# Optimization experiments

Hardware: AMD Instinct MI355X
Metric: run time of the kernel (lower is better)

Reference implementation:

```python
import jax, jax.numpy as jnp
import numpy as np

WINDOW = 2
OUT = 256


def setup_inputs() -> dict:
    key = jax.random.key(0)
    k1, k2 = jax.random.split(key)
    B, S, I = 8, 4096, 256
    x = jax.random.normal(k1, (B, S, I), dtype=jnp.float32)
    # fc: Linear(window*input -> 2*out*3)
    fan_in = WINDOW * I
    W_fc = jax.random.normal(k2, (2 * OUT * 3, fan_in), dtype=jnp.float32) / np.sqrt(fan_in)
    b_fc = jnp.zeros((2 * OUT * 3,), dtype=jnp.float32)
    return {"x": x, "W_fc": W_fc, "b_fc": b_fc}


def _forget_mult(z_t, f_t, reverse):
    # z_t, f_t: (S, B, O) time-major. c[t] = f[t]*c[prev] + (1-f[t])*z[t], c init 0.
    def step(c, fz):
        f, z = fz
        c = f * c + (1.0 - f) * z
        return c, c

    _, cs = jax.lax.scan(step, jnp.zeros_like(z_t[0]), (f_t, z_t), reverse=reverse)
    return cs  # (S, B, O)


def reference(x, W_fc, b_fc):
    B, S, I = x.shape
    pad = max(WINDOW - 1, 1)
    # stride(): left zero-pad then window of consecutive timesteps, flattened
    xp = jnp.pad(x, ((0, 0), (pad, 0), (0, 0)))
    win = jnp.concatenate([xp[:, k:k + S, :] for k in range(WINDOW)], axis=-1)  # (B,S,W*I)
    g = jnp.einsum('bsi,gi->bsg', win, W_fc) + b_fc  # (B,S,6*O)
    z, f, o = jnp.split(g, 3, axis=2)  # each (B,S,2*O)
    z = jnp.tanh(z)
    f = jax.nn.sigmoid(f)
    # time-major per-direction views
    zt = jnp.swapaxes(z.reshape(B, S, 2, OUT), 0, 1)  # (S,B,2,O)
    ft = jnp.swapaxes(f.reshape(B, S, 2, OUT), 0, 1)
    c_fwd = _forget_mult(zt[:, :, 0], ft[:, :, 0], reverse=False)
    c_bwd = _forget_mult(zt[:, :, 1], ft[:, :, 1], reverse=True)
    c = jnp.stack([c_fwd, c_bwd], axis=2)  # (S,B,2,O)
    c = jnp.swapaxes(c, 0, 1).reshape(B, S, 2 * OUT)
    return jax.nn.sigmoid(o) * c
```

## Files before the change

### kernel.cpp

```cpp
#include <hip/hip_runtime.h>
#include <hip/hip_bf16.h>
#include <stdint.h>

#define B_DIM 8
#define S_DIM 4096
#define I_DIM 256
#define M_DIM (B_DIM * S_DIM)
#define N_DIM 1536
#define K_DIM 512

#define TM 128
#define TN 128
#define BK 64

typedef __attribute__((ext_vector_type(8))) short bf16x8;
typedef __attribute__((ext_vector_type(4))) float f32x4;

typedef const void __attribute__((address_space(1)))* gas_ptr;
typedef void __attribute__((address_space(3)))* las_ptr;

__device__ __forceinline__ void gload_lds16(const void* g, void* l) {
    __builtin_amdgcn_global_load_lds((gas_ptr)(uintptr_t)g, (las_ptr)(uintptr_t)l, 16, 0, 0);
}

__device__ __forceinline__ float fast_sigmoid(float x) {
    return 1.0f / (1.0f + __expf(-x));
}
__device__ __forceinline__ float fast_tanh(float x) {
    float ax = fabsf(x);
    float e = __expf(-2.0f * ax);
    float t = (1.0f - e) / (1.0f + e);
    return copysignf(t, x);
}

__device__ __forceinline__ unsigned short f2bf(float f) {
    uint32_t u = __float_as_uint(f);
    uint32_t r = (u + 0x7FFFu + ((u >> 16) & 1u)) >> 16;
    return (unsigned short)r;
}

__global__ __launch_bounds__(256)
void cvt_f32_bf16(const float* __restrict__ in, unsigned short* __restrict__ out,
                  int n4, unsigned short* __restrict__ zp)
{
    int i = blockIdx.x * 256 + threadIdx.x;
    if (zp && blockIdx.x == 0 && threadIdx.x < 64) zp[threadIdx.x] = 0;
    if (i < n4) {
        float4 v = ((const float4*)in)[i];
        ushort4 o;
        o.x = f2bf(v.x); o.y = f2bf(v.y); o.z = f2bf(v.z); o.w = f2bf(v.w);
        ((ushort4*)out)[i] = o;
    }
}

__global__ __launch_bounds__(256, 2)
void qrnn_gemm(const __hip_bfloat16* __restrict__ x,
               const __hip_bfloat16* __restrict__ W,
               const float* __restrict__ bias,
               __hip_bfloat16* __restrict__ gact,
               const __hip_bfloat16* __restrict__ zeroPage)
{
    __shared__ __hip_bfloat16 lA[TM * BK];
    __shared__ __hip_bfloat16 lB[TN * BK];

    const int tid = threadIdx.x;
    const int w = tid >> 6;
    const int l = tid & 63;

    const int tileM = blockIdx.x & 255;
    const int tileN = blockIdx.x >> 8;
    const int m0 = tileM * TM;
    const int n0 = tileN * TN;
    const int bIdx = m0 >> 12;
    const int sBase = m0 & 4095;

    const int c8 = (l & 7) ^ ((l >> 3) & 7);
    const int rowInP = w * 8 + (l >> 3);

    const int la = l & 15, lq = l >> 4;
    const int wm = w >> 1, wn = w & 1;

    f32x4 acc[4][4] = {};

    for (int kt = 0; kt < K_DIM / BK; ++kt) {
        __syncthreads();
        const int kcol = kt * 64 + c8 * 8;
#pragma unroll
        for (int p = 0; p < 4; ++p) {
            const int r = p * 32 + rowInP;
            const int srow = sBase + r;
            const __hip_bfloat16* srcA;
            if (kcol < 256) {
                srcA = (srow == 0) ? zeroPage
                     : x + ((size_t)((bIdx << 12) + srow - 1) * 256 + kcol);
            } else {
                srcA = x + ((size_t)((bIdx << 12) + srow) * 256 + (kcol - 256));
            }
            gload_lds16(srcA, &lA[p * 2048 + w * 512]);
            const int nrow = n0 + r;
            gload_lds16(W + ((size_t)nrow * 512 + kcol), &lB[p * 2048 + w * 512]);
        }
        __syncthreads();

#pragma unroll
        for (int kk = 0; kk < 2; ++kk) {
            bf16x8 af[4], bfr[4];
#pragma unroll
            for (int i = 0; i < 4; ++i) {
                const int ra = wm * 64 + i * 16 + la;
                const int ch = (kk * 4 + lq) ^ (ra & 7);
                af[i] = *(const bf16x8*)&lA[ra * 64 + ch * 8];
            }
#pragma unroll
            for (int j = 0; j < 4; ++j) {
                const int rb = wn * 64 + j * 16 + la;
                const int ch = (kk * 4 + lq) ^ (rb & 7);
                bfr[j] = *(const bf16x8*)&lB[rb * 64 + ch * 8];
            }
#pragma unroll
            for (int i = 0; i < 4; ++i)
#pragma unroll
                for (int j = 0; j < 4; ++j)
                    acc[i][j] = __builtin_amdgcn_mfma_f32_16x16x32_bf16(
                        af[i], bfr[j], acc[i][j], 0, 0, 0);
        }
    }

    const int gate = n0 >> 9;
#pragma unroll
    for (int i = 0; i < 4; ++i) {
        const int mrow = m0 + wm * 64 + i * 16 + lq * 4;
#pragma unroll
        for (int j = 0; j < 4; ++j) {
            const int col = n0 + wn * 64 + j * 16 + la;
            const float bv = bias[col];
#pragma unroll
            for (int rr = 0; rr < 4; ++rr) {
                float v = acc[i][j][rr] + bv;
                float a = (gate == 0) ? fast_tanh(v) : fast_sigmoid(v);
                gact[(size_t)(mrow + rr) * N_DIM + col] = __float2bfloat16(a);
            }
        }
    }
}

#define NCHUNK 64
#define CLEN 64
#define NSEQ 4096

__global__ __launch_bounds__(256)
void qrnn_scanA(const __hip_bfloat16* __restrict__ gact,
                float* __restrict__ cA, float* __restrict__ cB)
{
    const int oo = threadIdx.x;
    const int bid = blockIdx.x;
    const int chunk = bid & 63;
    const int dir = (bid >> 6) & 1;
    const int b = bid >> 7;
    const int zc = dir * 256 + oo;
    const int t0 = chunk * CLEN;

    float A = 1.0f, Bv = 0.0f;
#pragma unroll 4
    for (int tt = 0; tt < CLEN; ++tt) {
        const int t = dir ? (t0 + CLEN - 1 - tt) : (t0 + tt);
        const size_t off = ((size_t)(b * S_DIM + t)) * N_DIM;
        const float z = __bfloat162float(gact[off + zc]);
        const float f = __bfloat162float(gact[off + 512 + zc]);
        Bv = f * Bv + (1.0f - f) * z;
        A *= f;
    }
    const int seq = (b * 2 + dir) * 256 + oo;
    cA[chunk * NSEQ + seq] = A;
    cB[chunk * NSEQ + seq] = Bv;
}

__global__ __launch_bounds__(256)
void qrnn_scanB(const float* __restrict__ cA, const float* __restrict__ cB,
                float* __restrict__ carry)
{
    const int seq = blockIdx.x * 256 + threadIdx.x;
    const int dir = (seq >> 8) & 1;
    float c = 0.0f;
    if (dir == 0) {
#pragma unroll 4
        for (int ch = 0; ch < NCHUNK; ++ch) {
            carry[ch * NSEQ + seq] = c;
            c = cA[ch * NSEQ + seq] * c + cB[ch * NSEQ + seq];
        }
    } else {
#pragma unroll 4
        for (int ch = NCHUNK - 1; ch >= 0; --ch) {
            carry[ch * NSEQ + seq] = c;
            c = cA[ch * NSEQ + seq] * c + cB[ch * NSEQ + seq];
        }
    }
}

__global__ __launch_bounds__(256)
void qrnn_scanC(const __hip_bfloat16* __restrict__ gact,
                const float* __restrict__ carry,
                float* __restrict__ out)
{
    const int oo = threadIdx.x;
    const int bid = blockIdx.x;
    const int chunk = bid & 63;
    const int dir = (bid >> 6) & 1;
    const int b = bid >> 7;
    const int zc = dir * 256 + oo;
    const int seq = (b * 2 + dir) * 256 + oo;
    const int t0 = chunk * CLEN;

    float c = carry[chunk * NSEQ + seq];
#pragma unroll 4
    for (int tt = 0; tt < CLEN; ++tt) {
        const int t = dir ? (t0 + CLEN - 1 - tt) : (t0 + tt);
        const size_t row = (size_t)(b * S_DIM + t);
        const size_t off = row * N_DIM;
        const float z = __bfloat162float(gact[off + zc]);
        const float f = __bfloat162float(gact[off + 512 + zc]);
        const float o = __bfloat162float(gact[off + 1024 + zc]);
        c = f * c + (1.0f - f) * z;
        out[row * 512 + zc] = o * c;
    }
}

extern "C" void kernel_launch(void* const* d_in, const int* in_sizes, int n_in,
                              void* d_out, int out_size, void* d_ws, size_t ws_size,
                              hipStream_t stream)
{
    const float* x    = (const float*)d_in[0];
    const float* W    = (const float*)d_in[1];
    const float* bias = (const float*)d_in[2];
    float* out = (float*)d_out;

    char* ws = (char*)d_ws;
    size_t off = 0;
    __hip_bfloat16* xb   = (__hip_bfloat16*)(ws + off); off += (size_t)M_DIM * I_DIM * 2;
    __hip_bfloat16* Wb   = (__hip_bfloat16*)(ws + off); off += (size_t)N_DIM * K_DIM * 2;
    __hip_bfloat16* gact = (__hip_bfloat16*)(ws + off); off += (size_t)M_DIM * N_DIM * 2;
    float* cA    = (float*)(ws + off); off += (size_t)NSEQ * NCHUNK * 4;
    float* cB    = (float*)(ws + off); off += (size_t)NSEQ * NCHUNK * 4;
    float* carry = (float*)(ws + off); off += (size_t)NSEQ * NCHUNK * 4;
    unsigned short* zeroPage = (unsigned short*)(ws + off); off += 128;

    const int nx4 = (M_DIM * I_DIM) / 4;
    const int nw4 = (N_DIM * K_DIM) / 4;
    cvt_f32_bf16<<<dim3((nx4 + 255) / 256), dim3(256), 0, stream>>>(x, (unsigned short*)xb, nx4, zeroPage);
    cvt_f32_bf16<<<dim3((nw4 + 255) / 256), dim3(256), 0, stream>>>(W, (unsigned short*)Wb, nw4, nullptr);

    qrnn_gemm<<<dim3(256 * 12), dim3(256), 0, stream>>>(xb, Wb, bias, gact,
                                                        (const __hip_bfloat16*)zeroPage);
    qrnn_scanA<<<dim3(B_DIM * 2 * NCHUNK), dim3(256), 0, stream>>>(gact, cA, cB);
    qrnn_scanB<<<dim3(NSEQ / 256), dim3(256), 0, stream>>>(cA, cB, carry);
    qrnn_scanC<<<dim3(B_DIM * 2 * NCHUNK), dim3(256), 0, stream>>>(gact, carry, out);
}
```

Measured before the change: 212.0 us.

## Store pre-activation gates transposed in fp16 and apply activations in scans

The GEMM epilogue now writes raw pre-activation gate values in fp16 to a column-major (gate-channel by time) buffer with 4-wide vector stores, and no longer applies tanh/sigmoid there. The scan kernels read contiguous 8-element fp16 vectors along time per channel and compute tanh/sigmoid themselves. The intent is to replace strided scalar gathers in the scans with wide contiguous loads. In exchange, scanA and scanC both recompute the activations, the GEMM stores become scattered across columns, and the output writes in scanC stay strided.

```diff
diff --git a/kernel.cpp b/kernel.cpp
--- a/kernel.cpp
+++ b/kernel.cpp
@@ -15,6 +15,8 @@
 
 typedef __attribute__((ext_vector_type(8))) short bf16x8;
 typedef __attribute__((ext_vector_type(4))) float f32x4;
+typedef _Float16 h4 __attribute__((ext_vector_type(4)));
+typedef _Float16 h8 __attribute__((ext_vector_type(8)));
 
 typedef const void __attribute__((address_space(1)))* gas_ptr;
 typedef void __attribute__((address_space(3)))* las_ptr;
@@ -57,7 +59,7 @@
 void qrnn_gemm(const __hip_bfloat16* __restrict__ x,
                const __hip_bfloat16* __restrict__ W,
                const float* __restrict__ bias,
-               __hip_bfloat16* __restrict__ gact,
+               _Float16* __restrict__ gT,
                const __hip_bfloat16* __restrict__ zeroPage)
 {
     __shared__ __hip_bfloat16 lA[TM * BK];
@@ -126,20 +128,18 @@
         }
     }
 
-    const int gate = n0 >> 9;
-#pragma unroll
-    for (int i = 0; i < 4; ++i) {
-        const int mrow = m0 + wm * 64 + i * 16 + lq * 4;
-#pragma unroll
-        for (int j = 0; j < 4; ++j) {
-            const int col = n0 + wn * 64 + j * 16 + la;
-            const float bv = bias[col];
-#pragma unroll
-            for (int rr = 0; rr < 4; ++rr) {
-                float v = acc[i][j][rr] + bv;
-                float a = (gate == 0) ? fast_tanh(v) : fast_sigmoid(v);
-                gact[(size_t)(mrow + rr) * N_DIM + col] = __float2bfloat16(a);
-            }
+#pragma unroll
+    for (int j = 0; j < 4; ++j) {
+        const int col = n0 + wn * 64 + j * 16 + la;
+        const float bv = bias[col];
+        _Float16* dst = gT + (size_t)col * 32768 + m0 + wm * 64 + lq * 4;
+#pragma unroll
+        for (int i = 0; i < 4; ++i) {
+            h4 hv;
+#pragma unroll
+            for (int rr = 0; rr < 4; ++rr)
+                hv[rr] = (_Float16)(acc[i][j][rr] + bv);
+            *(h4*)(dst + i * 16) = hv;
         }
     }
 }
@@ -149,7 +149,7 @@
 #define NSEQ 4096
 
 __global__ __launch_bounds__(256)
-void qrnn_scanA(const __hip_bfloat16* __restrict__ gact,
+void qrnn_scanA(const _Float16* __restrict__ gT,
                 float* __restrict__ cA, float* __restrict__ cB)
 {
     const int oo = threadIdx.x;
@@ -157,18 +157,36 @@
     const int chunk = bid & 63;
     const int dir = (bid >> 6) & 1;
     const int b = bid >> 7;
-    const int zc = dir * 256 + oo;
-    const int t0 = chunk * CLEN;
+
+    const size_t base = (size_t)(dir * 256 + oo) * 32768 + (b << 12) + chunk * CLEN;
+    const h8* zp = (const h8*)(gT + base);
+    const h8* fp = (const h8*)(gT + ((size_t)512 * 32768) + base);
 
     float A = 1.0f, Bv = 0.0f;
-#pragma unroll 4
-    for (int tt = 0; tt < CLEN; ++tt) {
-        const int t = dir ? (t0 + CLEN - 1 - tt) : (t0 + tt);
-        const size_t off = ((size_t)(b * S_DIM + t)) * N_DIM;
-        const float z = __bfloat162float(gact[off + zc]);
-        const float f = __bfloat162float(gact[off + 512 + zc]);
-        Bv = f * Bv + (1.0f - f) * z;
-        A *= f;
+    if (dir == 0) {
+#pragma unroll
+        for (int v = 0; v < 8; ++v) {
+            h8 zv = zp[v], fv = fp[v];
+#pragma unroll
+            for (int e = 0; e < 8; ++e) {
+                float f = fast_sigmoid((float)fv[e]);
+                float z = fast_tanh((float)zv[e]);
+                Bv = f * Bv + (1.0f - f) * z;
+                A *= f;
+            }
+        }
+    } else {
+#pragma unroll
+        for (int v = 7; v >= 0; --v) {
+            h8 zv = zp[v], fv = fp[v];
+#pragma unroll
+            for (int e = 7; e >= 0; --e) {
+                float f = fast_sigmoid((float)fv[e]);
+                float z = fast_tanh((float)zv[e]);
+                Bv = f * Bv + (1.0f - f) * z;
+                A *= f;
+            }
+        }
     }
     const int seq = (b * 2 + dir) * 256 + oo;
     cA[chunk * NSEQ + seq] = A;
@@ -198,7 +216,7 @@
 }
 
 __global__ __launch_bounds__(256)
-void qrnn_scanC(const __hip_bfloat16* __restrict__ gact,
+void qrnn_scanC(const _Float16* __restrict__ gT,
                 const float* __restrict__ carry,
                 float* __restrict__ out)
 {
@@ -211,17 +229,40 @@
     const int seq = (b * 2 + dir) * 256 + oo;
     const int t0 = chunk * CLEN;
 
+    const size_t base = (size_t)zc * 32768 + (b << 12) + t0;
+    const h8* zp = (const h8*)(gT + base);
+    const h8* fp = (const h8*)(gT + ((size_t)512 * 32768) + base);
+    const h8* op = (const h8*)(gT + ((size_t)1024 * 32768) + base);
+
     float c = carry[chunk * NSEQ + seq];
-#pragma unroll 4
-    for (int tt = 0; tt < CLEN; ++tt) {
-        const int t = dir ? (t0 + CLEN - 1 - tt) : (t0 + tt);
-        const size_t row = (size_t)(b * S_DIM + t);
-        const size_t off = row * N_DIM;
-        const float z = __bfloat162float(gact[off + zc]);
-        const float f = __bfloat162float(gact[off + 512 + zc]);
-        const float o = __bfloat162float(gact[off + 1024 + zc]);
-        c = f * c + (1.0f - f) * z;
-        out[row * 512 + zc] = o * c;
+    if (dir == 0) {
+#pragma unroll
+        for (int v = 0; v < 8; ++v) {
+            h8 zv = zp[v], fv = fp[v], ov = op[v];
+#pragma unroll
+            for (int e = 0; e < 8; ++e) {
+                float f = fast_sigmoid((float)fv[e]);
+                float z = fast_tanh((float)zv[e]);
+                float o = fast_sigmoid((float)ov[e]);
+                c = f * c + (1.0f - f) * z;
+                const int t = t0 + v * 8 + e;
+                out[((size_t)((b << 12) + t)) * 512 + zc] = o * c;
+            }
+        }
+    } else {
+#pragma unroll
+        for (int v = 7; v >= 0; --v) {
+            h8 zv = zp[v], fv = fp[v], ov = op[v];
+#pragma unroll
+            for (int e = 7; e >= 0; --e) {
+                float f = fast_sigmoid((float)fv[e]);
+                float z = fast_tanh((float)zv[e]);
+                float o = fast_sigmoid((float)ov[e]);
+                c = f * c + (1.0f - f) * z;
+                const int t = t0 + v * 8 + e;
+                out[((size_t)((b << 12) + t)) * 512 + zc] = o * c;
+            }
+        }
     }
 }
 
@@ -236,9 +277,9 @@
 
     char* ws = (char*)d_ws;
     size_t off = 0;
-    __hip_bfloat16* xb   = (__hip_bfloat16*)(ws + off); off += (size_t)M_DIM * I_DIM * 2;
-    __hip_bfloat16* Wb   = (__hip_bfloat16*)(ws + off); off += (size_t)N_DIM * K_DIM * 2;
-    __hip_bfloat16* gact = (__hip_bfloat16*)(ws + off); off += (size_t)M_DIM * N_DIM * 2;
+    __hip_bfloat16* xb = (__hip_bfloat16*)(ws + off); off += (size_t)M_DIM * I_DIM * 2;
+    __hip_bfloat16* Wb = (__hip_bfloat16*)(ws + off); off += (size_t)N_DIM * K_DIM * 2;
+    _Float16* gT = (_Float16*)(ws + off); off += (size_t)N_DIM * M_DIM * 2;
     float* cA    = (float*)(ws + off); off += (size_t)NSEQ * NCHUNK * 4;
     float* cB    = (float*)(ws + off); off += (size_t)NSEQ * NCHUNK * 4;
     float* carry = (float*)(ws + off); off += (size_t)NSEQ * NCHUNK * 4;
@@ -249,9 +290,9 @@
     cvt_f32_bf16<<<dim3((nx4 + 255) / 256), dim3(256), 0, stream>>>(x, (unsigned short*)xb, nx4, zeroPage);
     cvt_f32_bf16<<<dim3((nw4 + 255) / 256), dim3(256), 0, stream>>>(W, (unsigned short*)Wb, nw4, nullptr);
 
-    qrnn_gemm<<<dim3(256 * 12), dim3(256), 0, stream>>>(xb, Wb, bias, gact,
+    qrnn_gemm<<<dim3(256 * 12), dim3(256), 0, stream>>>(xb, Wb, bias, gT,
                                                         (const __hip_bfloat16*)zeroPage);
-    qrnn_scanA<<<dim3(B_DIM * 2 * NCHUNK), dim3(256), 0, stream>>>(gact, cA, cB);
+    qrnn_scanA<<<dim3(B_DIM * 2 * NCHUNK), dim3(256), 0, stream>>>(gT, cA, cB);
     qrnn_scanB<<<dim3(NSEQ / 256), dim3(256), 0, stream>>>(cA, cB, carry);
-    qrnn_scanC<<<dim3(B_DIM * 2 * NCHUNK), dim3(256), 0, stream>>>(gact, carry, out);
-}
+    qrnn_scanC<<<dim3(B_DIM * 2 * NCHUNK), dim3(256), 0, stream>>>(gT, carry, out);
+}
```

New measurement: 311.2 us. 1.47x slower.

## Store raw fp16 pre-activations with permuted columns; move activations into vectorized scans

Applied to the files above, without the earlier changes.

The GEMM epilogue now writes raw pre-activation values as fp16 rather than activated bf16. It permutes the W row loads so each lane owns 4 contiguous output columns and can issue 8-byte vector stores. The scan kernels now apply tanh and sigmoid themselves, each thread handles 4 channels with vector loads and stores, and the chunk count doubles to 128 with length 32. The aim is coalesced wide memory accesses and a lighter GEMM epilogue, at the cost of recomputing the activations in both scanA and scanC and of fp16 range limits on the pre-activations.

```diff
diff --git a/kernel.cpp b/kernel.cpp
--- a/kernel.cpp
+++ b/kernel.cpp
@@ -13,8 +13,13 @@
 #define TN 128
 #define BK 64
 
+#define NCHUNK 128
+#define CLEN 32
+#define NSEQ 4096
+
 typedef __attribute__((ext_vector_type(8))) short bf16x8;
 typedef __attribute__((ext_vector_type(4))) float f32x4;
+typedef _Float16 h4 __attribute__((ext_vector_type(4)));
 
 typedef const void __attribute__((address_space(1)))* gas_ptr;
 typedef void __attribute__((address_space(3)))* las_ptr;
@@ -57,7 +62,7 @@
 void qrnn_gemm(const __hip_bfloat16* __restrict__ x,
                const __hip_bfloat16* __restrict__ W,
                const float* __restrict__ bias,
-               __hip_bfloat16* __restrict__ gact,
+               _Float16* __restrict__ gact,
                const __hip_bfloat16* __restrict__ zeroPage)
 {
     __shared__ __hip_bfloat16 lA[TM * BK];
@@ -97,8 +102,8 @@
                 srcA = x + ((size_t)((bIdx << 12) + srow) * 256 + (kcol - 256));
             }
             gload_lds16(srcA, &lA[p * 2048 + w * 512]);
-            const int nrow = n0 + r;
-            gload_lds16(W + ((size_t)nrow * 512 + kcol), &lB[p * 2048 + w * 512]);
+            const int nr = (r & 64) + ((r & 15) << 2) + ((r >> 4) & 3);
+            gload_lds16(W + ((size_t)(n0 + nr) * 512 + kcol), &lB[p * 2048 + w * 512]);
         }
         __syncthreads();
 
@@ -126,53 +131,55 @@
         }
     }
 
-    const int gate = n0 >> 9;
+    const int colBase = n0 + wn * 64 + la * 4;
+    const float4 bv4 = *(const float4*)(bias + colBase);
 #pragma unroll
     for (int i = 0; i < 4; ++i) {
-        const int mrow = m0 + wm * 64 + i * 16 + lq * 4;
-#pragma unroll
-        for (int j = 0; j < 4; ++j) {
-            const int col = n0 + wn * 64 + j * 16 + la;
-            const float bv = bias[col];
-#pragma unroll
-            for (int rr = 0; rr < 4; ++rr) {
-                float v = acc[i][j][rr] + bv;
-                float a = (gate == 0) ? fast_tanh(v) : fast_sigmoid(v);
-                gact[(size_t)(mrow + rr) * N_DIM + col] = __float2bfloat16(a);
-            }
-        }
-    }
-}
-
-#define NCHUNK 64
-#define CLEN 64
-#define NSEQ 4096
-
-__global__ __launch_bounds__(256)
-void qrnn_scanA(const __hip_bfloat16* __restrict__ gact,
+        const int row0 = m0 + wm * 64 + i * 16 + lq * 4;
+#pragma unroll
+        for (int rr = 0; rr < 4; ++rr) {
+            h4 hv;
+            hv[0] = (_Float16)(acc[i][0][rr] + bv4.x);
+            hv[1] = (_Float16)(acc[i][1][rr] + bv4.y);
+            hv[2] = (_Float16)(acc[i][2][rr] + bv4.z);
+            hv[3] = (_Float16)(acc[i][3][rr] + bv4.w);
+            *(h4*)(gact + (size_t)(row0 + rr) * N_DIM + colBase) = hv;
+        }
+    }
+}
+
+__global__ __launch_bounds__(256)
+void qrnn_scanA(const _Float16* __restrict__ gact,
                 float* __restrict__ cA, float* __restrict__ cB)
 {
-    const int oo = threadIdx.x;
-    const int bid = blockIdx.x;
-    const int chunk = bid & 63;
-    const int dir = (bid >> 6) & 1;
-    const int b = bid >> 7;
-    const int zc = dir * 256 + oo;
+    const int c4  = threadIdx.x & 63;
+    const int chs = threadIdx.x >> 6;
+    const int cp  = blockIdx.x & 31;
+    const int dir = (blockIdx.x >> 5) & 1;
+    const int b   = blockIdx.x >> 6;
+    const int chunk = cp * 4 + chs;
+    const int zc = dir * 256 + c4 * 4;
     const int t0 = chunk * CLEN;
 
-    float A = 1.0f, Bv = 0.0f;
-#pragma unroll 4
+    float A[4] = {1.f, 1.f, 1.f, 1.f};
+    float Bv[4] = {0.f, 0.f, 0.f, 0.f};
+#pragma unroll 8
     for (int tt = 0; tt < CLEN; ++tt) {
         const int t = dir ? (t0 + CLEN - 1 - tt) : (t0 + tt);
-        const size_t off = ((size_t)(b * S_DIM + t)) * N_DIM;
-        const float z = __bfloat162float(gact[off + zc]);
-        const float f = __bfloat162float(gact[off + 512 + zc]);
-        Bv = f * Bv + (1.0f - f) * z;
-        A *= f;
-    }
-    const int seq = (b * 2 + dir) * 256 + oo;
-    cA[chunk * NSEQ + seq] = A;
-    cB[chunk * NSEQ + seq] = Bv;
+        const _Float16* rowp = gact + (size_t)((b << 12) + t) * N_DIM + zc;
+        h4 zv = *(const h4*)(rowp);
+        h4 fv = *(const h4*)(rowp + 512);
+#pragma unroll
+        for (int e = 0; e < 4; ++e) {
+            float f = fast_sigmoid((float)fv[e]);
+            float z = fast_tanh((float)zv[e]);
+            Bv[e] = f * Bv[e] + (1.0f - f) * z;
+            A[e] *= f;
+        }
+    }
+    const int seq0 = (b * 2 + dir) * 256 + c4 * 4;
+    *(float4*)(cA + (size_t)chunk * NSEQ + seq0) = make_float4(A[0], A[1], A[2], A[3]);
+    *(float4*)(cB + (size_t)chunk * NSEQ + seq0) = make_float4(Bv[0], Bv[1], Bv[2], Bv[3]);
 }
 
 __global__ __launch_bounds__(256)
@@ -198,30 +205,41 @@
 }
 
 __global__ __launch_bounds__(256)
-void qrnn_scanC(const __hip_bfloat16* __restrict__ gact,
+void qrnn_scanC(const _Float16* __restrict__ gact,
                 const float* __restrict__ carry,
                 float* __restrict__ out)
 {
-    const int oo = threadIdx.x;
-    const int bid = blockIdx.x;
-    const int chunk = bid & 63;
-    const int dir = (bid >> 6) & 1;
-    const int b = bid >> 7;
-    const int zc = dir * 256 + oo;
-    const int seq = (b * 2 + dir) * 256 + oo;
+    const int c4  = threadIdx.x & 63;
+    const int chs = threadIdx.x >> 6;
+    const int cp  = blockIdx.x & 31;
+    const int dir = (blockIdx.x >> 5) & 1;
+    const int b   = blockIdx.x >> 6;
+    const int chunk = cp * 4 + chs;
+    const int zc = dir * 256 + c4 * 4;
     const int t0 = chunk * CLEN;
-
-    float c = carry[chunk * NSEQ + seq];
-#pragma unroll 4
+    const int seq0 = (b * 2 + dir) * 256 + c4 * 4;
+
+    float4 cv = *(const float4*)(carry + (size_t)chunk * NSEQ + seq0);
+    float c[4] = {cv.x, cv.y, cv.z, cv.w};
+#pragma unroll 8
     for (int tt = 0; tt < CLEN; ++tt) {
         const int t = dir ? (t0 + CLEN - 1 - tt) : (t0 + tt);
-        const size_t row = (size_t)(b * S_DIM + t);
-        const size_t off = row * N_DIM;
-        const float z = __bfloat162float(gact[off + zc]);
-        const float f = __bfloat162float(gact[off + 512 + zc]);
-        const float o = __bfloat162float(gact[off + 1024 + zc]);
-        c = f * c + (1.0f - f) * z;
-        out[row * 512 + zc] = o * c;
+        const size_t row = (size_t)((b << 12) + t);
+        const _Float16* rowp = gact + row * N_DIM + zc;
+        h4 zv = *(const h4*)(rowp);
+        h4 fv = *(const h4*)(rowp + 512);
+        h4 ov = *(const h4*)(rowp + 1024);
+        float4 res;
+        float* rp = &res.x;
+#pragma unroll
+        for (int e = 0; e < 4; ++e) {
+            float f = fast_sigmoid((float)fv[e]);
+            float z = fast_tanh((float)zv[e]);
+            float o = fast_sigmoid((float)ov[e]);
+            c[e] = f * c[e] + (1.0f - f) * z;
+            rp[e] = o * c[e];
+        }
+        *(float4*)(out + row * 512 + zc) = res;
     }
 }
 
@@ -236,9 +254,9 @@
 
     char* ws = (char*)d_ws;
     size_t off = 0;
-    __hip_bfloat16* xb   = (__hip_bfloat16*)(ws + off); off += (size_t)M_DIM * I_DIM * 2;
-    __hip_bfloat16* Wb   = (__hip_bfloat16*)(ws + off); off += (size_t)N_DIM * K_DIM * 2;
-    __hip_bfloat16* gact = (__hip_bfloat16*)(ws + off); off += (size_t)M_DIM * N_DIM * 2;
+    __hip_bfloat16* xb = (__hip_bfloat16*)(ws + off); off += (size_t)M_DIM * I_DIM * 2;
+    __hip_bfloat16* Wb = (__hip_bfloat16*)(ws + off); off += (size_t)N_DIM * K_DIM * 2;
+    _Float16* gact = (_Float16*)(ws + off); off += (size_t)M_DIM * N_DIM * 2;
     float* cA    = (float*)(ws + off); off += (size_t)NSEQ * NCHUNK * 4;
     float* cB    = (float*)(ws + off); off += (size_t)NSEQ * NCHUNK * 4;
     float* carry = (float*)(ws + off); off += (size_t)NSEQ * NCHUNK * 4;
@@ -251,7 +269,7 @@
 
     qrnn_gemm<<<dim3(256 * 12), dim3(256), 0, stream>>>(xb, Wb, bias, gact,
                                                         (const __hip_bfloat16*)zeroPage);
-    qrnn_scanA<<<dim3(B_DIM * 2 * NCHUNK), dim3(256), 0, stream>>>(gact, cA, cB);
+    qrnn_scanA<<<dim3(512), dim3(256), 0, stream>>>(gact, cA, cB);
     qrnn_scanB<<<dim3(NSEQ / 256), dim3(256), 0, stream>>>(cA, cB, carry);
-    qrnn_scanC<<<dim3(B_DIM * 2 * NCHUNK), dim3(256), 0, stream>>>(gact, carry, out);
-}
+    qrnn_scanC<<<dim3(512), dim3(256), 0, stream>>>(gact, carry, out);
+}
```

After: 224.7 us. 6.0% more time.
